# Kernel optimization log

Hardware: AMD Instinct MI355X
Metric: run time of the kernel (lower is better)

## Reference

```python
import jax, jax.numpy as jnp
import numpy as np

N_TYPES = 4   # num_e_type+1 == num_n_type+1 == 4
N_HEAD = 8
D_K = 32
D_V = 32
NEG = -1e10


def setup_inputs() -> dict:
    key = jax.random.key(0)
    ks = jax.random.split(key, 16)
    B, N, D = 4096, 32, 256
    HK = N_HEAD * D_K
    s = 1.0 / np.sqrt(D)  # xavier-ish scale
    inp = {
        "q": jax.random.normal(ks[0], (B, N, D), jnp.float32),
        "k": jax.random.normal(ks[1], (B, N, D), jnp.float32),
        "v": jax.random.normal(ks[2], (B, N, D), jnp.float32),
        "Wq": jax.random.normal(ks[3], (N_TYPES, D, HK), jnp.float32) * s,
        "Wk": jax.random.normal(ks[4], (N_TYPES, D, HK), jnp.float32) * s,
        "Wv": jax.random.normal(ks[5], (N_TYPES, D, N_HEAD * D_V), jnp.float32) * s,
        "rel_pri": jax.random.uniform(ks[6], (N_TYPES, N_TYPES), jnp.float32, 0.5, 1.5),
        "fc_w": jax.random.normal(ks[7], (N_TYPES, N_HEAD * D_V, D), jnp.float32) * s,
        "fc_b": jax.random.normal(ks[8], (N_TYPES, D), jnp.float32) * 0.01,
        "gamma": jnp.ones((D,), jnp.float32),
        "beta": jnp.zeros((D,), jnp.float32),
        "seq_etype": jax.random.randint(ks[9], (B, N), 0, N_TYPES, jnp.int32),
        "seq_utype": jax.random.randint(ks[10], (B,), 0, N_TYPES, jnp.int32),
        "mask": jax.random.randint(ks[11], (B, N), 0, 2, jnp.int32).astype(bool),
    }
    return inp


def reference(q, k, v, Wq, Wk, Wv, rel_pri, fc_w, fc_b, gamma, beta,
              seq_etype, seq_utype, mask):
    B, N, D = q.shape
    temp = jnp.asarray(np.sqrt(D_K), q.dtype)

    # type-routed QKV projections: each (b,n) element uses weight of its edge type.
    # Equivalent to torch's sum over masked projections (no bias -> zeros project to 0).
    Q = jnp.zeros((B, N, N_HEAD * D_K), q.dtype)
    K = jnp.zeros((B, N, N_HEAD * D_K), q.dtype)
    V = jnp.zeros((B, N, N_HEAD * D_V), q.dtype)
    for e in range(N_TYPES):
        m = (seq_etype == e)[..., None]
        Q = Q + jnp.where(m, q, 0.0) @ Wq[e]
        K = K + jnp.where(m, k, 0.0) @ Wk[e]
        V = V + jnp.where(m, v, 0.0) @ Wv[e]

    Qh = Q.reshape(B, N, N_HEAD, D_K)
    Kh = K.reshape(B, N, N_HEAD, D_K)
    Vh = V.reshape(B, N, N_HEAD, D_V)

    # elementwise-dot attention scores [B, H, N]
    scores = jnp.einsum('bnhk,bnhk->bhn', Qh, Kh)
    pri = rel_pri[seq_utype[:, None], seq_etype]  # [B, N]
    scores = scores * pri[:, None, :] / temp
    scores = jnp.where(mask[:, None, :], NEG, scores)
    attn = jax.nn.softmax(scores, axis=-1)  # [B, H, N]

    # weighted neighbor sum -> [B, H*D_V] (head-major, matches torch view/transpose)
    out = jnp.einsum('bhn,bnhd->bhd', attn, Vh).reshape(B, N_HEAD * D_V)

    # type-routed output projection per src-node type
    proj = jnp.zeros((B, D), q.dtype)
    for u in range(N_TYPES):
        m = (seq_utype == u)[:, None]
        proj = proj + jnp.where(m, out @ fc_w[u] + fc_b[u], 0.0)

    # layer norm (eps = 1e-5 as torch default); dropout is identity in eval.
    mu = proj.mean(-1, keepdims=True)
    var = proj.var(-1, keepdims=True)
    normed = (proj - mu) * jax.lax.rsqrt(var + 1e-5) * gamma + beta

    attn_flat = attn.transpose(1, 0, 2).reshape(N_HEAD * B, N)  # torch layout [H*B, N]
    return normed, attn_flat
```

## Files before the change

kernel.cpp:

```cpp
#include <hip/hip_runtime.h>
#include <math.h>

namespace {
constexpr int Bt = 4096;
constexpr int Nt = 32;
constexpr int Dm = 256;
constexpr int NHEAD = 8;
constexpr float NEGV = -10000000000.0f;
constexpr int ATTN_BASE = Bt * Dm;
constexpr float INV_TEMP = 0.17677669529663687f;

__device__ __forceinline__ void project(const float* __restrict__ W, int j,
                                        const unsigned* tm,
                                        const float (*xs)[Dm],
                                        float* acc)
{
#pragma unroll
    for (int n = 0; n < Nt; ++n) acc[n] = 0.f;
#pragma unroll
    for (int e = 0; e < 4; ++e) {
        unsigned m = tm[e];
        if (m == 0) continue;
        const float* We = W + e * (Dm * Dm) + j;
        for (int d0 = 0; d0 < Dm; d0 += 16) {
            float w[16];
#pragma unroll
            for (int dd = 0; dd < 16; ++dd) w[dd] = We[(d0 + dd) * Dm];
#pragma unroll
            for (int n = 0; n < Nt; ++n) {
                if (m & (1u << n)) {
#pragma unroll
                    for (int c = 0; c < 4; ++c) {
                        float4 xv = *(const float4*)&xs[n][d0 + c * 4];
                        acc[n] = fmaf(xv.x, w[c * 4 + 0], acc[n]);
                        acc[n] = fmaf(xv.y, w[c * 4 + 1], acc[n]);
                        acc[n] = fmaf(xv.z, w[c * 4 + 2], acc[n]);
                        acc[n] = fmaf(xv.w, w[c * 4 + 3], acc[n]);
                    }
                }
            }
        }
    }
}
}

__global__ __launch_bounds__(256)
void mha_fused_kernel(const float* __restrict__ q, const float* __restrict__ k,
                      const float* __restrict__ v,
                      const float* __restrict__ Wq, const float* __restrict__ Wk,
                      const float* __restrict__ Wv,
                      const float* __restrict__ rel_pri,
                      const float* __restrict__ fc_w, const float* __restrict__ fc_b,
                      const float* __restrict__ gamma, const float* __restrict__ beta,
                      const int* __restrict__ seq_etype, const int* __restrict__ seq_utype,
                      const int* __restrict__ mask,
                      float* __restrict__ out)
{
    const int b = blockIdx.x;
    const int j = threadIdx.x;
    const int h = j >> 5;
    const int l = j & 31;

    __shared__ __align__(16) float xs[Nt][Dm];
    __shared__ __align__(16) float outbuf[Dm];
    __shared__ float attn_s[NHEAD][Nt];
    __shared__ float pri_s[Nt];
    __shared__ int   msks[Nt];
    __shared__ unsigned tmask_s[4];
    __shared__ int   ut_s;
    __shared__ float redA[4], redB[4];

    if (j < 4) tmask_s[j] = 0u;
    if (j == 0) ut_s = seq_utype[b];
    __syncthreads();
    if (j < Nt) {
        int e = seq_etype[b * Nt + j];
        msks[j] = mask[b * Nt + j];
        pri_s[j] = rel_pri[ut_s * 4 + e] * INV_TEMP;
        atomicOr(&tmask_s[e], 1u << j);
    }
    __syncthreads();

    unsigned tm[4];
#pragma unroll
    for (int e = 0; e < 4; ++e) tm[e] = __builtin_amdgcn_readfirstlane(tmask_s[e]);
    const int ut = __builtin_amdgcn_readfirstlane(ut_s);

    {
        const float4* s4 = (const float4*)(q + (size_t)b * (Nt * Dm));
        float4* d4 = (float4*)&xs[0][0];
#pragma unroll
        for (int r = 0; r < 8; ++r) d4[r * 256 + j] = s4[r * 256 + j];
    }
    __syncthreads();
    float Qacc[Nt];
    project(Wq, j, tm, xs, Qacc);
    __syncthreads();

    {
        const float4* s4 = (const float4*)(k + (size_t)b * (Nt * Dm));
        float4* d4 = (float4*)&xs[0][0];
#pragma unroll
        for (int r = 0; r < 8; ++r) d4[r * 256 + j] = s4[r * 256 + j];
    }
    __syncthreads();
    float Kacc[Nt];
    project(Wk, j, tm, xs, Kacc);

    float sc = 0.f;
#pragma unroll
    for (int n = 0; n < Nt; ++n) {
        float p = Qacc[n] * Kacc[n];
#pragma unroll
        for (int off = 16; off >= 1; off >>= 1) p += __shfl_xor(p, off, 64);
        sc = (l == n) ? p : sc;
    }

    sc = sc * pri_s[l];
    if (msks[l] != 0) sc = NEGV;
    float mx = sc;
#pragma unroll
    for (int off = 16; off >= 1; off >>= 1) mx = fmaxf(mx, __shfl_xor(mx, off, 64));
    float ex = expf(sc - mx);
    float sum = ex;
#pragma unroll
    for (int off = 16; off >= 1; off >>= 1) sum += __shfl_xor(sum, off, 64);
    float at = ex / sum;
    attn_s[h][l] = at;
    out[ATTN_BASE + h * (Bt * Nt) + b * Nt + l] = at;

    __syncthreads();
    {
        const float4* s4 = (const float4*)(v + (size_t)b * (Nt * Dm));
        float4* d4 = (float4*)&xs[0][0];
#pragma unroll
        for (int r = 0; r < 8; ++r) d4[r * 256 + j] = s4[r * 256 + j];
    }
    __syncthreads();
    float Vacc[Nt];
    project(Wv, j, tm, xs, Vacc);

    float o = 0.f;
#pragma unroll
    for (int n = 0; n < Nt; ++n) o = fmaf(attn_s[h][n], Vacc[n], o);
    outbuf[j] = o;
    __syncthreads();

    const float* Wf = fc_w + ut * (Dm * Dm) + j;
    float pj = fc_b[ut * Dm + j];
    for (int i0 = 0; i0 < Dm; i0 += 4) {
        float4 ov = *(const float4*)&outbuf[i0];
        pj = fmaf(ov.x, Wf[(i0 + 0) * Dm], pj);
        pj = fmaf(ov.y, Wf[(i0 + 1) * Dm], pj);
        pj = fmaf(ov.z, Wf[(i0 + 2) * Dm], pj);
        pj = fmaf(ov.w, Wf[(i0 + 3) * Dm], pj);
    }

    float s1 = pj, s2 = pj * pj;
#pragma unroll
    for (int off = 32; off >= 1; off >>= 1) {
        s1 += __shfl_xor(s1, off, 64);
        s2 += __shfl_xor(s2, off, 64);
    }
    const int w = j >> 6;
    if ((j & 63) == 0) { redA[w] = s1; redB[w] = s2; }
    __syncthreads();
    float t1 = redA[0] + redA[1] + redA[2] + redA[3];
    float t2 = redB[0] + redB[1] + redB[2] + redB[3];
    float mu = t1 * (1.f / 256.f);
    float var = t2 * (1.f / 256.f) - mu * mu;
    float inv = rsqrtf(var + 1e-5f);
    out[b * Dm + j] = (pj - mu) * inv * gamma[j] + beta[j];
}

extern "C" void kernel_launch(void* const* d_in, const int* in_sizes, int n_in,
                              void* d_out, int out_size, void* d_ws, size_t ws_size,
                              hipStream_t stream) {
    const float* q       = (const float*)d_in[0];
    const float* k       = (const float*)d_in[1];
    const float* v       = (const float*)d_in[2];
    const float* Wq      = (const float*)d_in[3];
    const float* Wk      = (const float*)d_in[4];
    const float* Wv      = (const float*)d_in[5];
    const float* rel_pri = (const float*)d_in[6];
    const float* fc_w    = (const float*)d_in[7];
    const float* fc_b    = (const float*)d_in[8];
    const float* gamma   = (const float*)d_in[9];
    const float* beta    = (const float*)d_in[10];
    const int* seq_etype = (const int*)d_in[11];
    const int* seq_utype = (const int*)d_in[12];
    const int* mask      = (const int*)d_in[13];
    float* outp = (float*)d_out;

    mha_fused_kernel<<<Bt, 256, 0, stream>>>(q, k, v, Wq, Wk, Wv, rel_pri,
                                             fc_w, fc_b, gamma, beta,
                                             seq_etype, seq_utype, mask, outp);
}
```

Baseline: 1.334 ms.

## Double block to 512 threads, computing Q and K projections concurrently in two groups

The block grows to 512 threads. The first 256 compute the Q projection while the second 256 compute K at the same time, staging q and k in halves of the feature dimension so both fit in shared memory. The V projection is split by token across the two groups, and the fc projection is split by input dimension with a partial-sum reduction through shared memory. This is meant to raise parallelism and latency hiding per block, at the cost of more barriers, register pressure from the launch-bounds hint, and repeated reads of the weights per half.

Result: slower. 1.766 ms (+32.4%).

```diff
diff --git a/kernel.cpp b/kernel.cpp
--- a/kernel.cpp
+++ b/kernel.cpp
@@ -5,33 +5,33 @@
 constexpr int Bt = 4096;
 constexpr int Nt = 32;
 constexpr int Dm = 256;
+constexpr int DH = 128;
 constexpr int NHEAD = 8;
 constexpr float NEGV = -10000000000.0f;
 constexpr int ATTN_BASE = Bt * Dm;
 constexpr float INV_TEMP = 0.17677669529663687f;
 
-__device__ __forceinline__ void project(const float* __restrict__ W, int j,
-                                        const unsigned* tm,
-                                        const float (*xs)[Dm],
-                                        float* acc)
+template <int NTOK>
+__device__ __forceinline__ void project_half(const float* __restrict__ W, int j,
+                                             const unsigned* tm,
+                                             const float (*xs)[DH], int rowbase,
+                                             int tokbase, float* acc)
 {
-#pragma unroll
-    for (int n = 0; n < Nt; ++n) acc[n] = 0.f;
 #pragma unroll
     for (int e = 0; e < 4; ++e) {
         unsigned m = tm[e];
         if (m == 0) continue;
-        const float* We = W + e * (Dm * Dm) + j;
-        for (int d0 = 0; d0 < Dm; d0 += 16) {
+        const float* We = W + e * (Dm * Dm) + rowbase * Dm + j;
+        for (int d0 = 0; d0 < DH; d0 += 16) {
             float w[16];
 #pragma unroll
             for (int dd = 0; dd < 16; ++dd) w[dd] = We[(d0 + dd) * Dm];
 #pragma unroll
-            for (int n = 0; n < Nt; ++n) {
+            for (int n = 0; n < NTOK; ++n) {
                 if (m & (1u << n)) {
 #pragma unroll
                     for (int c = 0; c < 4; ++c) {
-                        float4 xv = *(const float4*)&xs[n][d0 + c * 4];
+                        float4 xv = *(const float4*)&xs[tokbase + n][d0 + c * 4];
                         acc[n] = fmaf(xv.x, w[c * 4 + 0], acc[n]);
                         acc[n] = fmaf(xv.y, w[c * 4 + 1], acc[n]);
                         acc[n] = fmaf(xv.z, w[c * 4 + 2], acc[n]);
@@ -44,7 +44,7 @@
 }
 }
 
-__global__ __launch_bounds__(256)
+__global__ __launch_bounds__(512, 8)
 void mha_fused_kernel(const float* __restrict__ q, const float* __restrict__ k,
                       const float* __restrict__ v,
                       const float* __restrict__ Wq, const float* __restrict__ Wk,
@@ -57,12 +57,15 @@
                       float* __restrict__ out)
 {
     const int b = blockIdx.x;
-    const int j = threadIdx.x;
+    const int t = threadIdx.x;
+    const int j = t & 255;
+    const int grp = t >> 8;
     const int h = j >> 5;
     const int l = j & 31;
 
-    __shared__ __align__(16) float xs[Nt][Dm];
-    __shared__ __align__(16) float outbuf[Dm];
+    __shared__ __align__(16) float smem[2 * Nt * DH];
+    __shared__ __align__(16) float outbuf[2][Dm];
+    __shared__ __align__(16) float fcpart[2][Dm];
     __shared__ float attn_s[NHEAD][Nt];
     __shared__ float pri_s[Nt];
     __shared__ int   msks[Nt];
@@ -70,14 +73,18 @@
     __shared__ int   ut_s;
     __shared__ float redA[4], redB[4];
 
-    if (j < 4) tmask_s[j] = 0u;
-    if (j == 0) ut_s = seq_utype[b];
-    __syncthreads();
-    if (j < Nt) {
-        int e = seq_etype[b * Nt + j];
-        msks[j] = mask[b * Nt + j];
-        pri_s[j] = rel_pri[ut_s * 4 + e] * INV_TEMP;
-        atomicOr(&tmask_s[e], 1u << j);
+    float (*xsA)[DH] = (float(*)[DH])smem;
+    float (*xsB)[DH] = (float(*)[DH])(smem + Nt * DH);
+    float (*Klds)[Dm] = (float(*)[Dm])smem;
+
+    if (t < 4) tmask_s[t] = 0u;
+    if (t == 0) ut_s = seq_utype[b];
+    __syncthreads();
+    if (t < Nt) {
+        int e = seq_etype[b * Nt + t];
+        msks[t] = mask[b * Nt + t];
+        pri_s[t] = rel_pri[ut_s * 4 + e] * INV_TEMP;
+        atomicOr(&tmask_s[e], 1u << t);
     }
     __syncthreads();
 
@@ -86,91 +93,128 @@
     for (int e = 0; e < 4; ++e) tm[e] = __builtin_amdgcn_readfirstlane(tmask_s[e]);
     const int ut = __builtin_amdgcn_readfirstlane(ut_s);
 
+    const float4* sq = (const float4*)(q + (size_t)b * (Nt * Dm));
+    const float4* sk = (const float4*)(k + (size_t)b * (Nt * Dm));
+    float4* dA = (float4*)smem;
+    float4* dB = dA + (Nt * DH / 4);
+
+    const float* Wsel = grp ? Wk : Wq;
+    const float (*xsel)[DH] = grp ? xsB : xsA;
+
+    float acc[Nt];
+#pragma unroll
+    for (int n = 0; n < Nt; ++n) acc[n] = 0.f;
+
+#pragma unroll
+    for (int half = 0; half < 2; ++half) {
+#pragma unroll
+        for (int r = 0; r < 2; ++r) {
+            int t4 = r * 512 + t;
+            int n = t4 >> 5, c = t4 & 31;
+            dA[t4] = sq[n * 64 + half * 32 + c];
+            dB[t4] = sk[n * 64 + half * 32 + c];
+        }
+        __syncthreads();
+        project_half<Nt>(Wsel, j, tm, xsel, half * DH, 0, acc);
+        __syncthreads();
+    }
+
+    if (grp) {
+#pragma unroll
+        for (int n = 0; n < Nt; ++n) Klds[n][j] = acc[n];
+    }
+    __syncthreads();
+
+    if (!grp) {
+        float sc = 0.f;
+#pragma unroll
+        for (int n = 0; n < Nt; ++n) {
+            float p = acc[n] * Klds[n][j];
+#pragma unroll
+            for (int off = 16; off >= 1; off >>= 1) p += __shfl_xor(p, off, 64);
+            sc = (l == n) ? p : sc;
+        }
+        sc = sc * pri_s[l];
+        if (msks[l] != 0) sc = NEGV;
+        float mx = sc;
+#pragma unroll
+        for (int off = 16; off >= 1; off >>= 1) mx = fmaxf(mx, __shfl_xor(mx, off, 64));
+        float ex = expf(sc - mx);
+        float sum = ex;
+#pragma unroll
+        for (int off = 16; off >= 1; off >>= 1) sum += __shfl_xor(sum, off, 64);
+        float at = ex / sum;
+        attn_s[h][l] = at;
+        out[ATTN_BASE + h * (Bt * Nt) + b * Nt + l] = at;
+    }
+    __syncthreads();
+
+    const float4* sv = (const float4*)(v + (size_t)b * (Nt * Dm));
+    unsigned tmv[4];
+#pragma unroll
+    for (int e = 0; e < 4; ++e) tmv[e] = grp ? (tm[e] >> 16) : (tm[e] & 0xFFFFu);
+    const int tokbase = grp ? 16 : 0;
+
+    float vacc[16];
+#pragma unroll
+    for (int n = 0; n < 16; ++n) vacc[n] = 0.f;
+
+#pragma unroll
+    for (int half = 0; half < 2; ++half) {
+#pragma unroll
+        for (int r = 0; r < 2; ++r) {
+            int t4 = r * 512 + t;
+            int n = t4 >> 5, c = t4 & 31;
+            dA[t4] = sv[n * 64 + half * 32 + c];
+        }
+        __syncthreads();
+        project_half<16>(Wv, j, tmv, xsA, half * DH, tokbase, vacc);
+        __syncthreads();
+    }
+
+    float o = 0.f;
+#pragma unroll
+    for (int n = 0; n < 16; ++n) o = fmaf(attn_s[h][tokbase + n], vacc[n], o);
+    outbuf[grp][j] = o;
+    __syncthreads();
+
+    const float* Wf = fc_w + ut * (Dm * Dm) + j;
+    float pj = grp ? 0.f : fc_b[ut * Dm + j];
     {
-        const float4* s4 = (const float4*)(q + (size_t)b * (Nt * Dm));
-        float4* d4 = (float4*)&xs[0][0];
-#pragma unroll
-        for (int r = 0; r < 8; ++r) d4[r * 256 + j] = s4[r * 256 + j];
-    }
-    __syncthreads();
-    float Qacc[Nt];
-    project(Wq, j, tm, xs, Qacc);
-    __syncthreads();
-
-    {
-        const float4* s4 = (const float4*)(k + (size_t)b * (Nt * Dm));
-        float4* d4 = (float4*)&xs[0][0];
-#pragma unroll
-        for (int r = 0; r < 8; ++r) d4[r * 256 + j] = s4[r * 256 + j];
-    }
-    __syncthreads();
-    float Kacc[Nt];
-    project(Wk, j, tm, xs, Kacc);
-
-    float sc = 0.f;
-#pragma unroll
-    for (int n = 0; n < Nt; ++n) {
-        float p = Qacc[n] * Kacc[n];
-#pragma unroll
-        for (int off = 16; off >= 1; off >>= 1) p += __shfl_xor(p, off, 64);
-        sc = (l == n) ? p : sc;
-    }
-
-    sc = sc * pri_s[l];
-    if (msks[l] != 0) sc = NEGV;
-    float mx = sc;
-#pragma unroll
-    for (int off = 16; off >= 1; off >>= 1) mx = fmaxf(mx, __shfl_xor(mx, off, 64));
-    float ex = expf(sc - mx);
-    float sum = ex;
-#pragma unroll
-    for (int off = 16; off >= 1; off >>= 1) sum += __shfl_xor(sum, off, 64);
-    float at = ex / sum;
-    attn_s[h][l] = at;
-    out[ATTN_BASE + h * (Bt * Nt) + b * Nt + l] = at;
-
-    __syncthreads();
-    {
-        const float4* s4 = (const float4*)(v + (size_t)b * (Nt * Dm));
-        float4* d4 = (float4*)&xs[0][0];
-#pragma unroll
-        for (int r = 0; r < 8; ++r) d4[r * 256 + j] = s4[r * 256 + j];
-    }
-    __syncthreads();
-    float Vacc[Nt];
-    project(Wv, j, tm, xs, Vacc);
-
-    float o = 0.f;
-#pragma unroll
-    for (int n = 0; n < Nt; ++n) o = fmaf(attn_s[h][n], Vacc[n], o);
-    outbuf[j] = o;
-    __syncthreads();
-
-    const float* Wf = fc_w + ut * (Dm * Dm) + j;
-    float pj = fc_b[ut * Dm + j];
-    for (int i0 = 0; i0 < Dm; i0 += 4) {
-        float4 ov = *(const float4*)&outbuf[i0];
-        pj = fmaf(ov.x, Wf[(i0 + 0) * Dm], pj);
-        pj = fmaf(ov.y, Wf[(i0 + 1) * Dm], pj);
-        pj = fmaf(ov.z, Wf[(i0 + 2) * Dm], pj);
-        pj = fmaf(ov.w, Wf[(i0 + 3) * Dm], pj);
-    }
-
-    float s1 = pj, s2 = pj * pj;
-#pragma unroll
-    for (int off = 32; off >= 1; off >>= 1) {
-        s1 += __shfl_xor(s1, off, 64);
-        s2 += __shfl_xor(s2, off, 64);
-    }
-    const int w = j >> 6;
-    if ((j & 63) == 0) { redA[w] = s1; redB[w] = s2; }
-    __syncthreads();
-    float t1 = redA[0] + redA[1] + redA[2] + redA[3];
-    float t2 = redB[0] + redB[1] + redB[2] + redB[3];
-    float mu = t1 * (1.f / 256.f);
-    float var = t2 * (1.f / 256.f) - mu * mu;
-    float inv = rsqrtf(var + 1e-5f);
-    out[b * Dm + j] = (pj - mu) * inv * gamma[j] + beta[j];
+        const int ibase = grp * 128;
+        for (int i0 = 0; i0 < 128; i0 += 4) {
+            float4 a0 = *(const float4*)&outbuf[0][ibase + i0];
+            float4 a1 = *(const float4*)&outbuf[1][ibase + i0];
+            pj = fmaf(a0.x + a1.x, Wf[(ibase + i0 + 0) * Dm], pj);
+            pj = fmaf(a0.y + a1.y, Wf[(ibase + i0 + 1) * Dm], pj);
+            pj = fmaf(a0.z + a1.z, Wf[(ibase + i0 + 2) * Dm], pj);
+            pj = fmaf(a0.w + a1.w, Wf[(ibase + i0 + 3) * Dm], pj);
+        }
+    }
+    fcpart[grp][j] = pj;
+    __syncthreads();
+
+    float pjf = 0.f;
+    if (!grp) {
+        pjf = fcpart[0][j] + fcpart[1][j];
+        float s1 = pjf, s2 = pjf * pjf;
+#pragma unroll
+        for (int off = 32; off >= 1; off >>= 1) {
+            s1 += __shfl_xor(s1, off, 64);
+            s2 += __shfl_xor(s2, off, 64);
+        }
+        const int w = j >> 6;
+        if ((j & 63) == 0) { redA[w] = s1; redB[w] = s2; }
+    }
+    __syncthreads();
+    if (!grp) {
+        float t1 = redA[0] + redA[1] + redA[2] + redA[3];
+        float t2 = redB[0] + redB[1] + redB[2] + redB[3];
+        float mu = t1 * (1.f / 256.f);
+        float var = t2 * (1.f / 256.f) - mu * mu;
+        float inv = rsqrtf(var + 1e-5f);
+        out[b * Dm + j] = (pjf - mu) * inv * gamma[j] + beta[j];
+    }
 }
 
 extern "C" void kernel_launch(void* const* d_in, const int* in_sizes, int n_in,
@@ -192,7 +236,7 @@
     const int* mask      = (const int*)d_in[13];
     float* outp = (float*)d_out;
 
-    mha_fused_kernel<<<Bt, 256, 0, stream>>>(q, k, v, Wq, Wk, Wv, rel_pri,
+    mha_fused_kernel<<<Bt, 512, 0, stream>>>(q, k, v, Wq, Wk, Wv, rel_pri,
                                              fc_w, fc_b, gamma, beta,
                                              seq_etype, seq_utype, mask, outp);
 }
```
